# Performance work log

Hardware: AMD Instinct MI355X
Metric: run time of the kernel (lower is better)

## Reference

```python
import jax, jax.numpy as jnp
import numpy as np

DEPTH = 6
GAMMA = 1e-4
DIM = 1024
HIDDEN = 16
OUT_DIM = 64
N = 16384


def setup_inputs() -> dict:
    key = jax.random.key(0)
    k0, k1, k2, k3, k4 = jax.random.split(key, 5)
    X = jax.random.normal(k0, (N, DIM), dtype=jnp.float32)
    s1 = 1.0 / np.sqrt(DIM)
    s2 = 1.0 / np.sqrt(HIDDEN)
    W1 = jax.random.uniform(k1, (DIM, HIDDEN), jnp.float32, -s1, s1)
    b1 = jax.random.uniform(k2, (HIDDEN,), jnp.float32, -s1, s1)
    W2 = jax.random.uniform(k3, (HIDDEN, OUT_DIM), jnp.float32, -s2, s2)
    b2 = jax.random.uniform(k4, (OUT_DIM,), jnp.float32, -s2, s2)
    return {"X": X, "W1": W1, "b1": b1, "W2": W2, "b2": b2}


def _mlp(X, W1, b1, W2, b2):
    # shared FeedForwardClassifier: Linear(dim,16) -> ReLU -> Linear(16,out_dim)
    return jax.nn.relu(X @ W1 + b1) @ W2 + b2


def reference(X, W1, b1, W2, b2):
    for _ in range(DEPTH):
        # custom LayerNorm: row-wise L2 normalization (no eps in original)
        Xn = X / jnp.linalg.norm(X, axis=-1, keepdims=True)  # [N, dim]
        P = jax.nn.softmax(_mlp(Xn, W1, b1, W2, b2), axis=-1)  # [N, out_dim]
        # X + g*P@P.T@X - g*X@X.T@X, contracted small-Gram-first (same math)
        PtX = P.T @ Xn          # [out_dim, dim]
        G = Xn.T @ Xn           # [dim, dim]
        X = Xn + GAMMA * (P @ PtX) - GAMMA * (Xn @ G)
    return _mlp(X, W1, b1, W2, b2)
```

## Files before the change

### kernel.cpp

```cpp
#include <hip/hip_runtime.h>


#define N_ROWS 16384
#define DIM 1024
#define HID 16
#define OUTD 64
#define DEPTH 6
#define GAMMA 1e-4f

typedef short bf16x8 __attribute__((ext_vector_type(8)));
typedef unsigned short u16x8 __attribute__((ext_vector_type(8)));
typedef float f32x4 __attribute__((ext_vector_type(4)));

#define AS1C(p) ((const __attribute__((address_space(1))) void*)(p))
#define AS3(p)  ((__attribute__((address_space(3))) void*)(p))

__device__ __forceinline__ unsigned short f2bf(float f) {
    unsigned u = __builtin_bit_cast(unsigned, f);
    u += 0x7fffu + ((u >> 16) & 1u);
    return (unsigned short)(u >> 16);
}
__device__ __forceinline__ float b2f(ushort u) {
    unsigned x = ((unsigned)u) << 16;
    return __builtin_bit_cast(float, x);
}
__device__ __forceinline__ int swz(int n, int row) {
    return (n & ~63) | ((((n >> 3) & 7) ^ (row & 7)) << 3) | (n & 7);
}

__device__ __forceinline__ void atom_pk_bf16(ushort* p, ushort lo, ushort hi) {
#if __has_builtin(__builtin_amdgcn_global_atomic_fadd_v2bf16)
    typedef short s16x2 __attribute__((ext_vector_type(2)));
    s16x2 v;
    v[0] = (short)lo; v[1] = (short)hi;
    __builtin_amdgcn_global_atomic_fadd_v2bf16(
        (__attribute__((address_space(1))) s16x2*)p, v);
#else
    unsigned* up = (unsigned*)p;
    unsigned expected = *up;
    while (true) {
        float flo = b2f((ushort)(expected & 0xffffu)) + b2f(lo);
        float fhi = b2f((ushort)(expected >> 16)) + b2f(hi);
        unsigned desired = (unsigned)f2bf(flo) | ((unsigned)f2bf(fhi) << 16);
        unsigned old = atomicCAS(up, expected, desired);
        if (old == expected) break;
        expected = old;
    }
#endif
}

__global__ __launch_bounds__(256) void tobf16_k(const float* __restrict__ X,
        ushort* __restrict__ Xm, float* __restrict__ rinv) {
    int row = blockIdx.x, t = threadIdx.x;
    float4 v = ((const float4*)(X + (size_t)row * DIM))[t];
    ushort4 o4;
    o4.x = f2bf(v.x); o4.y = f2bf(v.y); o4.z = f2bf(v.z); o4.w = f2bf(v.w);
    *(ushort4*)(Xm + (size_t)row * DIM + swz(t * 4, row)) = o4;
    float ss = v.x * v.x + v.y * v.y + v.z * v.z + v.w * v.w;
    for (int o = 32; o > 0; o >>= 1) ss += __shfl_down(ss, o);
    __shared__ float wsum[4];
    if ((t & 63) == 0) wsum[t >> 6] = ss;
    __syncthreads();
    if (t == 0) rinv[row] = 1.0f / sqrtf(wsum[0] + wsum[1] + wsum[2] + wsum[3]);
}

__global__ __launch_bounds__(256) void rsqrt_k(const float* __restrict__ ssacc,
        float* __restrict__ rinv) {
    int i = blockIdx.x * 256 + threadIdx.x;
    rinv[i] = 1.0f / sqrtf(ssacc[i]);
}

__global__ __launch_bounds__(256) void transpose_k(const ushort* __restrict__ Xm,
        const float* __restrict__ rinv, ushort* __restrict__ XnT) {
    int r0 = blockIdx.x * 64;
    int c0 = blockIdx.y * 64;
    int t = threadIdx.x;
    __shared__ float ts[64 * 65];
    __shared__ float riS[64];
    if (t < 64) riS[t] = rinv[r0 + t];
    __syncthreads();
#pragma unroll
    for (int i = 0; i < 2; ++i) {
        int idx = i * 256 + t;
        int r = idx >> 3, lg = idx & 7;
        int rr = r0 + r;
        const ushort* p = Xm + (size_t)rr * DIM + c0 + ((lg ^ (rr & 7)) << 3);
        u16x8 a = *(const u16x8*)p;
        float s = riS[r];
        float* d = &ts[r * 65 + lg * 8];
#pragma unroll
        for (int u = 0; u < 8; ++u) d[u] = b2f(a[u]) * s;
    }
    __syncthreads();
#pragma unroll
    for (int i = 0; i < 2; ++i) {
        int g = i * 256 + t;
        int c = g >> 3;
        int rg = g & 7;
        u16x8 pk;
#pragma unroll
        for (int u = 0; u < 8; ++u) pk[u] = f2bf(ts[(rg * 8 + u) * 65 + c]);
        *(u16x8*)(XnT + (size_t)(c0 + c) * N_ROWS + r0 + ((rg ^ (c & 7)) << 3)) = pk;
    }
}

__global__ __launch_bounds__(256) void prep_w1t_k(const float* __restrict__ W1,
        ushort* __restrict__ W1T) {
    int idx = blockIdx.x * 256 + threadIdx.x;
    int h = idx >> 10, j = idx & 1023;
    W1T[idx] = f2bf(W1[j * HID + h]);
}

__global__ __launch_bounds__(256) void zgemm_k(const ushort* __restrict__ Xm,
        const ushort* __restrict__ W1T, const float* __restrict__ b1,
        float* __restrict__ z, const float* __restrict__ rv) {
    int t = threadIdx.x;
    int wave = t >> 6, lane = t & 63;
    int rl = lane & 15, q = lane >> 4;
    int rowbase = blockIdx.x * 64 + wave * 16;
    int m = rowbase + rl;
    int msw = m & 7;
    const ushort* arow = Xm + (size_t)m * DIM;
    const ushort* brow = W1T + (size_t)rl * DIM + q * 8;
    f32x4 acc = {0.f, 0.f, 0.f, 0.f};
#pragma unroll 8
    for (int kt = 0; kt < DIM; kt += 32) {
        int gl = ((kt >> 3) & 7) | q;
        int off = (kt & ~63) + ((gl ^ msw) << 3);
        bf16x8 a = *(const bf16x8*)(arow + off);
        bf16x8 b = *(const bf16x8*)(brow + kt);
        acc = __builtin_amdgcn_mfma_f32_16x16x32_bf16(a, b, acc, 0, 0, 0);
    }
#pragma unroll
    for (int rg = 0; rg < 4; ++rg) {
        int mm = rowbase + q * 4 + rg;
        float s = rv ? rv[mm] : 1.0f;
        z[(size_t)mm * HID + rl] = acc[rg] * s + b1[rl];
    }
}

__global__ __launch_bounds__(256) void head_k(const float* __restrict__ z,
        const float* __restrict__ W2, const float* __restrict__ b2,
        ushort* __restrict__ Pb, ushort* __restrict__ PTb,
        float* __restrict__ out, int do_softmax) {
    __shared__ float w2s[HID * OUTD];
    __shared__ float b2s[OUTD];
    int t = threadIdx.x;
    ((float4*)w2s)[t] = ((const float4*)W2)[t];
    if (t < OUTD) b2s[t] = b2[t];
    __syncthreads();
    int m = blockIdx.x * 256 + t;
    float h[HID];
    const float4* zp = (const float4*)(z + (size_t)m * HID);
#pragma unroll
    for (int i = 0; i < 4; ++i) {
        float4 v = zp[i];
        h[i * 4 + 0] = fmaxf(v.x, 0.f); h[i * 4 + 1] = fmaxf(v.y, 0.f);
        h[i * 4 + 2] = fmaxf(v.z, 0.f); h[i * 4 + 3] = fmaxf(v.w, 0.f);
    }
    float lo[OUTD];
#pragma unroll
    for (int o = 0; o < OUTD; ++o) lo[o] = b2s[o];
    for (int i = 0; i < HID; ++i) {
        float hv = h[i];
#pragma unroll
        for (int o = 0; o < OUTD; ++o) lo[o] += hv * w2s[i * OUTD + o];
    }
    if (do_softmax) {
        float mx = lo[0];
#pragma unroll
        for (int o = 1; o < OUTD; ++o) mx = fmaxf(mx, lo[o]);
        float sm = 0.f;
#pragma unroll
        for (int o = 0; o < OUTD; ++o) { float e = __expf(lo[o] - mx); lo[o] = e; sm += e; }
        float inv = 1.0f / sm;
#pragma unroll
        for (int o8 = 0; o8 < 8; ++o8) {
            u16x8 pk;
#pragma unroll
            for (int u = 0; u < 8; ++u) pk[u] = f2bf(lo[o8 * 8 + u] * inv);
            ((u16x8*)(Pb + (size_t)m * OUTD))[o8 ^ (m & 7)] = pk;
        }
#pragma unroll
        for (int o = 0; o < OUTD; ++o)
            PTb[(size_t)o * N_ROWS + swz(m, o)] = f2bf(lo[o] * inv);
    } else {
        float4* op = (float4*)(out + (size_t)m * OUTD);
#pragma unroll
        for (int o4 = 0; o4 < 16; ++o4) {
            float4 v; v.x = lo[o4 * 4 + 0]; v.y = lo[o4 * 4 + 1];
            v.z = lo[o4 * 4 + 2]; v.w = lo[o4 * 4 + 3];
            op[o4] = v;
        }
    }
}

__global__ __launch_bounds__(256) void castgp_k(const ushort* __restrict__ Gacc,
        const ushort* __restrict__ PtXacc, ushort* __restrict__ Gb,
        ushort* __restrict__ PtXTb) {
    int idx = blockIdx.x * 256 + threadIdx.x;
    if (idx < 262144) {
        int n = idx >> 8;
        int so = (idx & 255) * 4;
        int k0 = (so & ~63) | ((((so >> 3) & 7) ^ (n & 7)) << 3) | (so & 7);
        ushort4 o;
        ushort v0 = (k0 + 0 > n) ? Gacc[(size_t)n * DIM + k0 + 0] : Gacc[(size_t)(k0 + 0) * DIM + n];
        ushort v1 = (k0 + 1 > n) ? Gacc[(size_t)n * DIM + k0 + 1] : Gacc[(size_t)(k0 + 1) * DIM + n];
        ushort v2 = (k0 + 2 > n) ? Gacc[(size_t)n * DIM + k0 + 2] : Gacc[(size_t)(k0 + 2) * DIM + n];
        ushort v3 = (k0 + 3 > n) ? Gacc[(size_t)n * DIM + k0 + 3] : Gacc[(size_t)(k0 + 3) * DIM + n];
        o.x = v0 ^ 0x8000u; o.y = v1 ^ 0x8000u;
        o.z = v2 ^ 0x8000u; o.w = v3 ^ 0x8000u;
        *(ushort4*)(Gb + (size_t)n * DIM + so) = o;
    } else {
        int vv = idx - 262144;
        int d = vv >> 4;
        int so = (vv & 15) * 4;
        int k0 = ((((so >> 3) & 7) ^ (d & 7)) << 3) | (so & 7);
        const ushort* src = PtXacc + (size_t)d * OUTD + k0;
        ushort4 o;
        o.x = src[0]; o.y = src[1]; o.z = src[2]; o.w = src[3];
        *(ushort4*)(PtXTb + (size_t)d * OUTD + so) = o;
    }
}

template<int BM, int BN, int EPI, int TRI>
__global__ __launch_bounds__(256, 3) void gemm_nt_k(
        const ushort* __restrict__ A0, int lda0,
        const ushort* __restrict__ B0, int ldb0, int k0len,
        const ushort* __restrict__ A1, int lda1,
        const ushort* __restrict__ B1, int ldb1, int k1len,
        float* __restrict__ C, int ldc,
        const float* __restrict__ rinv, float gamma,
        float* __restrict__ ssacc) {
    constexpr int WTN = BN / 2;
    constexpr int NF = WTN / 16;
    constexpr int NAW = BM / 64;
    constexpr int NBW = BN / 64;
    __shared__ ushort ls[(BM + BN) * 64];
    ushort* lsA = ls;
    ushort* lsB = ls + BM * 64;
    int t = threadIdx.x;
    int wave = t >> 6, lane = t & 63;
    int rl = lane & 15, q = lane >> 4;
    int wm = wave & 1, wn = wave >> 1;
    int m0, n0, zidx;
    if (TRI) {
        int bid = blockIdx.x;
        int rest = bid >> 3;
        int bx = rest % 36, tm = 0;
        int zhi = rest / 36;
        zidx = (bid & 7) | (zhi << 3);
        while (bx >= 8 - tm) { bx -= 8 - tm; ++tm; }
        m0 = tm * 128; n0 = (tm + bx) * 128;
    } else {
        m0 = blockIdx.x * BM; n0 = blockIdx.y * BN; zidx = blockIdx.z;
    }
    int lrow8 = lane >> 3, lgrp = lane & 7;
    bool isA = wave < NAW;
    bool active = wave < NAW + NBW;
    int wlocal = isA ? wave : wave - NAW;
    ushort* dstb = ls + (isA ? 0 : BM * 64) + wlocal * 4096;

    f32x4 acc[4][NF];
#pragma unroll
    for (int i = 0; i < 4; ++i)
#pragma unroll
        for (int j = 0; j < NF; ++j) acc[i][j] = f32x4{0.f, 0.f, 0.f, 0.f};
    float rvv[4][4];

    for (int seg = 0; seg < 2; ++seg) {
        int klen = seg ? k1len : k0len;
        if (klen > 0) {
            const ushort* OPA = seg ? A1 : A0;
            const ushort* OPB = seg ? B1 : B0;
            int ldaS = seg ? lda1 : lda0;
            int ldbS = seg ? ldb1 : ldb0;
            int kb = seg ? 0 : zidx * k0len;
            const ushort* srcb;
            size_t ldS;
            if (isA) {
                srcb = OPA + (size_t)(m0 + wlocal * 64 + lrow8) * ldaS + lgrp * 8;
                ldS = (size_t)ldaS;
            } else {
                srcb = OPB + (size_t)(n0 + wlocal * 64 + lrow8) * ldbS + lgrp * 8;
                ldS = (size_t)ldbS;
            }
            srcb += kb;
            for (int kt = 0; kt < klen; kt += 64) {
                if (active) {
#pragma unroll
                    for (int c = 0; c < 8; ++c)
                        __builtin_amdgcn_global_load_lds(AS1C(srcb + c * 8 * ldS),
                                                         AS3(dstb + c * 512), 16, 0, 0);
                    srcb += 64;
                }
                __syncthreads();
#pragma unroll
                for (int s = 0; s < 2; ++s) {
                    bf16x8 af[4], bfr[NF];
#pragma unroll
                    for (int i = 0; i < 4; ++i) {
                        int row = wm * 64 + i * 16 + rl;
                        int sg = ((s << 2) | q) ^ (row & 7);
                        af[i] = *(const bf16x8*)&lsA[row * 64 + sg * 8];
                    }
#pragma unroll
                    for (int j = 0; j < NF; ++j) {
                        int row = wn * WTN + j * 16 + rl;
                        int sg = ((s << 2) | q) ^ (row & 7);
                        bfr[j] = *(const bf16x8*)&lsB[row * 64 + sg * 8];
                    }
#pragma unroll
                    for (int i = 0; i < 4; ++i)
#pragma unroll
                        for (int j = 0; j < NF; ++j)
                            acc[i][j] = __builtin_amdgcn_mfma_f32_16x16x32_bf16(
                                af[i], bfr[j], acc[i][j], 0, 0, 0);
                }
                __syncthreads();
            }
        }
        if (EPI == 1 && seg == 0) {
#pragma unroll
            for (int i = 0; i < 4; ++i)
#pragma unroll
                for (int rg = 0; rg < 4; ++rg)
                    rvv[i][rg] = rinv[m0 + wm * 64 + i * 16 + q * 4 + rg];
#pragma unroll
            for (int i = 0; i < 4; ++i)
#pragma unroll
                for (int j = 0; j < NF; ++j)
#pragma unroll
                    for (int rg = 0; rg < 4; ++rg)
                        acc[i][j][rg] *= rvv[i][rg];
        }
    }

    if (EPI == 0) {
        ushort* Cb = (ushort*)C;
#pragma unroll
        for (int i = 0; i < 4; ++i)
#pragma unroll
            for (int j = 0; j < NF; ++j)
#pragma unroll
                for (int rg = 0; rg < 4; ++rg) {
                    int m = m0 + wm * 64 + i * 16 + q * 4 + rg;
                    int n = n0 + wn * WTN + j * 16 + rl;
                    float v = acc[i][j][rg];
                    float vp = __shfl_xor(v, 1);
                    if ((rl & 1) == 0)
                        atom_pk_bf16(&Cb[(size_t)m * ldc + n], f2bf(v), f2bf(vp));
                }
    } else {
#pragma unroll
        for (int i = 0; i < 4; ++i)
#pragma unroll
            for (int rg = 0; rg < 4; ++rg) {
                int m = m0 + wm * 64 + i * 16 + q * 4 + rg;
                float ssl = 0.f;
#pragma unroll
                for (int j = 0; j < NF; ++j) {
                    int n = n0 + wn * WTN + j * 16 + rl;
                    int so = swz(n, m);
                    float base = b2f(A0[(size_t)m * lda0 + so]);
                    float vf = base * rvv[i][rg] + gamma * acc[i][j][rg];
                    ((ushort*)C)[(size_t)m * ldc + so] = f2bf(vf);
                    ssl += vf * vf;
                }
                ssl += __shfl_xor(ssl, 1);
                ssl += __shfl_xor(ssl, 2);
                ssl += __shfl_xor(ssl, 4);
                ssl += __shfl_xor(ssl, 8);
                if (rl == 0) atomicAdd(&ssacc[m], ssl);
            }
    }
}

extern "C" void kernel_launch(void* const* d_in, const int* in_sizes, int n_in,
                              void* d_out, int out_size, void* d_ws, size_t ws_size,
                              hipStream_t stream) {
    const float* X = (const float*)d_in[0];
    const float* W1 = (const float*)d_in[1];
    const float* b1 = (const float*)d_in[2];
    const float* W2 = (const float*)d_in[3];
    const float* b2 = (const float*)d_in[4];
    float* out = (float*)d_out;
    char* ws = (char*)d_ws;

    constexpr size_t O_BufA  = 0;
    constexpr size_t O_BufB  = O_BufA + (size_t)N_ROWS * DIM * 2;
    constexpr size_t O_Pb    = O_BufB + (size_t)N_ROWS * DIM * 2;
    constexpr size_t O_PTb   = O_Pb + (size_t)N_ROWS * OUTD * 2;
    constexpr size_t O_Gacc  = O_PTb + (size_t)OUTD * N_ROWS * 2;
    constexpr size_t O_PXacc = O_Gacc + (size_t)DIM * DIM * 2;
    constexpr size_t O_ssacc = O_PXacc + (size_t)DIM * OUTD * 2;
    constexpr size_t O_Gb    = O_ssacc + (size_t)N_ROWS * 4;
    constexpr size_t O_PtXTb = O_Gb + (size_t)DIM * DIM * 2;
    constexpr size_t O_riv   = O_PtXTb + (size_t)DIM * OUTD * 2;
    constexpr size_t O_z     = O_riv + (size_t)N_ROWS * 4;
    constexpr size_t O_W1T   = O_z + (size_t)N_ROWS * HID * 4;

    ushort* bufA  = (ushort*)(ws + O_BufA);
    ushort* bufB  = (ushort*)(ws + O_BufB);
    ushort* Pb    = (ushort*)(ws + O_Pb);
    ushort* PTb   = (ushort*)(ws + O_PTb);
    ushort* Gacc  = (ushort*)(ws + O_Gacc);
    ushort* PXacc = (ushort*)(ws + O_PXacc);
    float*  ssacc = (float*)(ws + O_ssacc);
    ushort* Gb    = (ushort*)(ws + O_Gb);
    ushort* PtXTb = (ushort*)(ws + O_PtXTb);
    float*  riv   = (float*)(ws + O_riv);
    float*  z     = (float*)(ws + O_z);
    ushort* W1T   = (ushort*)(ws + O_W1T);
    (void)in_sizes; (void)n_in; (void)out_size; (void)ws_size;

    prep_w1t_k<<<64, 256, 0, stream>>>(W1, W1T);
    tobf16_k<<<N_ROWS, 256, 0, stream>>>(X, bufA, riv);

    ushort* xm  = bufA;
    ushort* alt = bufB;

    for (int it = 0; it < DEPTH; ++it) {
        transpose_k<<<dim3(N_ROWS / 64, DIM / 64), 256, 0, stream>>>(xm, riv, alt);
        zgemm_k<<<N_ROWS / 64, 256, 0, stream>>>(xm, W1T, b1, z, riv);
        head_k<<<N_ROWS / 256, 256, 0, stream>>>(z, W2, b2, Pb, PTb, nullptr, 1);
        hipMemsetAsync(ws + O_Gacc, 0,
                       (size_t)DIM * DIM * 2 + (size_t)DIM * OUTD * 2
                       + (size_t)N_ROWS * 4, stream);
        gemm_nt_k<128, 128, 0, 1><<<dim3(8 * 36 * 2, 1, 1), 256, 0, stream>>>(
            alt, N_ROWS, alt, N_ROWS, 1024,
            nullptr, 0, nullptr, 0, 0,
            (float*)Gacc, DIM, nullptr, 0.f, nullptr);
        gemm_nt_k<128, 64, 0, 0><<<dim3(8, 1, 64), 256, 0, stream>>>(
            alt, N_ROWS, PTb, N_ROWS, 256,
            nullptr, 0, nullptr, 0, 0,
            (float*)PXacc, OUTD, nullptr, 0.f, nullptr);
        castgp_k<<<1088, 256, 0, stream>>>(Gacc, PXacc, Gb, PtXTb);
        gemm_nt_k<128, 128, 1, 0><<<dim3(N_ROWS / 128, DIM / 128, 1), 256, 0, stream>>>(
            xm, DIM, Gb, DIM, 1024,
            Pb, OUTD, PtXTb, OUTD, OUTD,
            (float*)alt, DIM, riv, GAMMA, ssacc);
        rsqrt_k<<<N_ROWS / 256, 256, 0, stream>>>(ssacc, riv);
        ushort* tmp = xm; xm = alt; alt = tmp;
    }

    zgemm_k<<<N_ROWS / 64, 256, 0, stream>>>(xm, W1T, b1, z, nullptr);
    head_k<<<N_ROWS / 256, 256, 0, stream>>>(z, W2, b2, Pb, PTb, out, 0);
}
```

Before: 1.088 ms.

## Merge Gram and PᵀX GEMMs into one launch and fuse zeroing into rsqrt

Replaces the two split-K accumulation GEMMs (XᵀX triangle and PᵀX) with one kernel launch of 1088 blocks, padding PT to 128 rows so both use 128x128 tiles. The per-iteration memset is removed: the rsqrt kernel now also clears ssacc and the Gacc/PXacc accumulators, and an initial memset covers the first iteration. The z buffer is aliased onto Gb. The goal is fewer launches and better load balance across one combined grid. The cost is extra padded PᵀX work, and correctness now depends on the aliasing and zeroing order.

Measured after the change: 1.129 ms. +3.7%, slower.

```diff
diff --git a/kernel.cpp b/kernel.cpp
--- a/kernel.cpp
+++ b/kernel.cpp
@@ -64,10 +64,14 @@
     if (t == 0) rinv[row] = 1.0f / sqrtf(wsum[0] + wsum[1] + wsum[2] + wsum[3]);
 }
 
-__global__ __launch_bounds__(256) void rsqrt_k(const float* __restrict__ ssacc,
-        float* __restrict__ rinv) {
+__global__ __launch_bounds__(256) void rsqrt_zero_k(float* __restrict__ ssacc,
+        float* __restrict__ rinv, uint4* __restrict__ gz) {
     int i = blockIdx.x * 256 + threadIdx.x;
-    rinv[i] = 1.0f / sqrtf(ssacc[i]);
+    if (i < N_ROWS) {
+        rinv[i] = 1.0f / sqrtf(ssacc[i]);
+        ssacc[i] = 0.f;
+    }
+    gz[i] = uint4{0u, 0u, 0u, 0u};
 }
 
 __global__ __launch_bounds__(256) void transpose_k(const ushort* __restrict__ Xm,
@@ -196,7 +200,7 @@
 }
 
 __global__ __launch_bounds__(256) void castgp_k(const ushort* __restrict__ Gacc,
-        const ushort* __restrict__ PtXacc, ushort* __restrict__ Gb,
+        const ushort* __restrict__ PXacc, ushort* __restrict__ Gb,
         ushort* __restrict__ PtXTb) {
     int idx = blockIdx.x * 256 + threadIdx.x;
     if (idx < 262144) {
@@ -216,111 +220,178 @@
         int d = vv >> 4;
         int so = (vv & 15) * 4;
         int k0 = ((((so >> 3) & 7) ^ (d & 7)) << 3) | (so & 7);
-        const ushort* src = PtXacc + (size_t)d * OUTD + k0;
+        const ushort* src = PXacc + (size_t)d * 128 + k0;
         ushort4 o;
         o.x = src[0]; o.y = src[1]; o.z = src[2]; o.w = src[3];
         *(ushort4*)(PtXTb + (size_t)d * OUTD + so) = o;
     }
 }
 
-template<int BM, int BN, int EPI, int TRI>
-__global__ __launch_bounds__(256, 3) void gemm_nt_k(
+__global__ __launch_bounds__(256, 3) void gemm_gp_k(
+        const ushort* __restrict__ XnT, const ushort* __restrict__ PTpad,
+        ushort* __restrict__ Gacc, ushort* __restrict__ PXacc) {
+    __shared__ ushort ls[256 * 64];
+    ushort* lsA = ls;
+    ushort* lsB = ls + 128 * 64;
+    int t = threadIdx.x;
+    int wave = t >> 6, lane = t & 63;
+    int rl = lane & 15, q = lane >> 4;
+    int wm = wave & 1, wn = wave >> 1;
+    int bid = blockIdx.x;
+    int m0, n0, kb, ksteps, ldc;
+    const ushort* B;
+    ushort* C;
+    if (bid < 576) {
+        int rest = bid >> 3;
+        int bx = rest % 36, zhi = rest / 36, tm = 0;
+        int zidx = (bid & 7) | (zhi << 3);
+        while (bx >= 8 - tm) { bx -= 8 - tm; ++tm; }
+        m0 = tm * 128; n0 = (tm + bx) * 128;
+        kb = zidx * 1024; ksteps = 16;
+        B = XnT; C = Gacc; ldc = DIM;
+    } else {
+        int b2 = bid - 576;
+        int zidx = b2 & 63;
+        m0 = (b2 >> 6) * 128; n0 = 0;
+        kb = zidx * 256; ksteps = 4;
+        B = PTpad; C = PXacc; ldc = 128;
+    }
+    int lrow8 = lane >> 3, lgrp = lane & 7;
+    bool isA = wave < 2;
+    int wlocal = wave & 1;
+    ushort* dstb = ls + (isA ? 0 : 8192) + wlocal * 4096;
+    const ushort* srcb = (isA
+        ? XnT + (size_t)(m0 + wlocal * 64 + lrow8) * N_ROWS
+        : B   + (size_t)(n0 + wlocal * 64 + lrow8) * N_ROWS) + kb + lgrp * 8;
+
+    f32x4 acc[4][4];
+#pragma unroll
+    for (int i = 0; i < 4; ++i)
+#pragma unroll
+        for (int j = 0; j < 4; ++j) acc[i][j] = f32x4{0.f, 0.f, 0.f, 0.f};
+
+    for (int st = 0; st < ksteps; ++st) {
+#pragma unroll
+        for (int c = 0; c < 8; ++c)
+            __builtin_amdgcn_global_load_lds(AS1C(srcb + (size_t)c * 8 * N_ROWS),
+                                             AS3(dstb + c * 512), 16, 0, 0);
+        srcb += 64;
+        __syncthreads();
+#pragma unroll
+        for (int s = 0; s < 2; ++s) {
+            bf16x8 af[4], bfr[4];
+#pragma unroll
+            for (int i = 0; i < 4; ++i) {
+                int row = wm * 64 + i * 16 + rl;
+                int sg = ((s << 2) | q) ^ (row & 7);
+                af[i] = *(const bf16x8*)&lsA[row * 64 + sg * 8];
+            }
+#pragma unroll
+            for (int j = 0; j < 4; ++j) {
+                int row = wn * 64 + j * 16 + rl;
+                int sg = ((s << 2) | q) ^ (row & 7);
+                bfr[j] = *(const bf16x8*)&lsB[row * 64 + sg * 8];
+            }
+#pragma unroll
+            for (int i = 0; i < 4; ++i)
+#pragma unroll
+                for (int j = 0; j < 4; ++j)
+                    acc[i][j] = __builtin_amdgcn_mfma_f32_16x16x32_bf16(
+                        af[i], bfr[j], acc[i][j], 0, 0, 0);
+        }
+        __syncthreads();
+    }
+
+#pragma unroll
+    for (int i = 0; i < 4; ++i)
+#pragma unroll
+        for (int j = 0; j < 4; ++j)
+#pragma unroll
+            for (int rg = 0; rg < 4; ++rg) {
+                int m = m0 + wm * 64 + i * 16 + q * 4 + rg;
+                int n = n0 + wn * 64 + j * 16 + rl;
+                float v = acc[i][j][rg];
+                float vp = __shfl_xor(v, 1);
+                if ((rl & 1) == 0)
+                    atom_pk_bf16(&C[(size_t)m * ldc + n], f2bf(v), f2bf(vp));
+            }
+}
+
+__global__ __launch_bounds__(256, 3) void gemm_upd_k(
         const ushort* __restrict__ A0, int lda0,
         const ushort* __restrict__ B0, int ldb0, int k0len,
         const ushort* __restrict__ A1, int lda1,
         const ushort* __restrict__ B1, int ldb1, int k1len,
-        float* __restrict__ C, int ldc,
+        ushort* __restrict__ C, int ldc,
         const float* __restrict__ rinv, float gamma,
         float* __restrict__ ssacc) {
-    constexpr int WTN = BN / 2;
-    constexpr int NF = WTN / 16;
-    constexpr int NAW = BM / 64;
-    constexpr int NBW = BN / 64;
-    __shared__ ushort ls[(BM + BN) * 64];
+    __shared__ ushort ls[256 * 64];
     ushort* lsA = ls;
-    ushort* lsB = ls + BM * 64;
+    ushort* lsB = ls + 128 * 64;
     int t = threadIdx.x;
     int wave = t >> 6, lane = t & 63;
     int rl = lane & 15, q = lane >> 4;
     int wm = wave & 1, wn = wave >> 1;
-    int m0, n0, zidx;
-    if (TRI) {
-        int bid = blockIdx.x;
-        int rest = bid >> 3;
-        int bx = rest % 36, tm = 0;
-        int zhi = rest / 36;
-        zidx = (bid & 7) | (zhi << 3);
-        while (bx >= 8 - tm) { bx -= 8 - tm; ++tm; }
-        m0 = tm * 128; n0 = (tm + bx) * 128;
-    } else {
-        m0 = blockIdx.x * BM; n0 = blockIdx.y * BN; zidx = blockIdx.z;
-    }
+    int m0 = blockIdx.x * 128, n0 = blockIdx.y * 128;
     int lrow8 = lane >> 3, lgrp = lane & 7;
-    bool isA = wave < NAW;
-    bool active = wave < NAW + NBW;
-    int wlocal = isA ? wave : wave - NAW;
-    ushort* dstb = ls + (isA ? 0 : BM * 64) + wlocal * 4096;
-
-    f32x4 acc[4][NF];
+    bool isA = wave < 2;
+    int wlocal = wave & 1;
+    ushort* dstb = ls + (isA ? 0 : 8192) + wlocal * 4096;
+
+    f32x4 acc[4][4];
 #pragma unroll
     for (int i = 0; i < 4; ++i)
 #pragma unroll
-        for (int j = 0; j < NF; ++j) acc[i][j] = f32x4{0.f, 0.f, 0.f, 0.f};
+        for (int j = 0; j < 4; ++j) acc[i][j] = f32x4{0.f, 0.f, 0.f, 0.f};
     float rvv[4][4];
 
     for (int seg = 0; seg < 2; ++seg) {
         int klen = seg ? k1len : k0len;
-        if (klen > 0) {
-            const ushort* OPA = seg ? A1 : A0;
-            const ushort* OPB = seg ? B1 : B0;
-            int ldaS = seg ? lda1 : lda0;
-            int ldbS = seg ? ldb1 : ldb0;
-            int kb = seg ? 0 : zidx * k0len;
-            const ushort* srcb;
-            size_t ldS;
-            if (isA) {
-                srcb = OPA + (size_t)(m0 + wlocal * 64 + lrow8) * ldaS + lgrp * 8;
-                ldS = (size_t)ldaS;
-            } else {
-                srcb = OPB + (size_t)(n0 + wlocal * 64 + lrow8) * ldbS + lgrp * 8;
-                ldS = (size_t)ldbS;
+        const ushort* OPA = seg ? A1 : A0;
+        const ushort* OPB = seg ? B1 : B0;
+        int ldaS = seg ? lda1 : lda0;
+        int ldbS = seg ? ldb1 : ldb0;
+        const ushort* srcb;
+        size_t ldS;
+        if (isA) {
+            srcb = OPA + (size_t)(m0 + wlocal * 64 + lrow8) * ldaS + lgrp * 8;
+            ldS = (size_t)ldaS;
+        } else {
+            srcb = OPB + (size_t)(n0 + wlocal * 64 + lrow8) * ldbS + lgrp * 8;
+            ldS = (size_t)ldbS;
+        }
+        for (int kt = 0; kt < klen; kt += 64) {
+#pragma unroll
+            for (int c = 0; c < 8; ++c)
+                __builtin_amdgcn_global_load_lds(AS1C(srcb + c * 8 * ldS),
+                                                 AS3(dstb + c * 512), 16, 0, 0);
+            srcb += 64;
+            __syncthreads();
+#pragma unroll
+            for (int s = 0; s < 2; ++s) {
+                bf16x8 af[4], bfr[4];
+#pragma unroll
+                for (int i = 0; i < 4; ++i) {
+                    int row = wm * 64 + i * 16 + rl;
+                    int sg = ((s << 2) | q) ^ (row & 7);
+                    af[i] = *(const bf16x8*)&lsA[row * 64 + sg * 8];
+                }
+#pragma unroll
+                for (int j = 0; j < 4; ++j) {
+                    int row = wn * 64 + j * 16 + rl;
+                    int sg = ((s << 2) | q) ^ (row & 7);
+                    bfr[j] = *(const bf16x8*)&lsB[row * 64 + sg * 8];
+                }
+#pragma unroll
+                for (int i = 0; i < 4; ++i)
+#pragma unroll
+                    for (int j = 0; j < 4; ++j)
+                        acc[i][j] = __builtin_amdgcn_mfma_f32_16x16x32_bf16(
+                            af[i], bfr[j], acc[i][j], 0, 0, 0);
             }
-            srcb += kb;
-            for (int kt = 0; kt < klen; kt += 64) {
-                if (active) {
-#pragma unroll
-                    for (int c = 0; c < 8; ++c)
-                        __builtin_amdgcn_global_load_lds(AS1C(srcb + c * 8 * ldS),
-                                                         AS3(dstb + c * 512), 16, 0, 0);
-                    srcb += 64;
-                }
-                __syncthreads();
-#pragma unroll
-                for (int s = 0; s < 2; ++s) {
-                    bf16x8 af[4], bfr[NF];
-#pragma unroll
-                    for (int i = 0; i < 4; ++i) {
-                        int row = wm * 64 + i * 16 + rl;
-                        int sg = ((s << 2) | q) ^ (row & 7);
-                        af[i] = *(const bf16x8*)&lsA[row * 64 + sg * 8];
-                    }
-#pragma unroll
-                    for (int j = 0; j < NF; ++j) {
-                        int row = wn * WTN + j * 16 + rl;
-                        int sg = ((s << 2) | q) ^ (row & 7);
-                        bfr[j] = *(const bf16x8*)&lsB[row * 64 + sg * 8];
-                    }
-#pragma unroll
-                    for (int i = 0; i < 4; ++i)
-#pragma unroll
-                        for (int j = 0; j < NF; ++j)
-                            acc[i][j] = __builtin_amdgcn_mfma_f32_16x16x32_bf16(
-                                af[i], bfr[j], acc[i][j], 0, 0, 0);
-                }
-                __syncthreads();
-            }
-        }
-        if (EPI == 1 && seg == 0) {
+            __syncthreads();
+        }
+        if (seg == 0) {
 #pragma unroll
             for (int i = 0; i < 4; ++i)
 #pragma unroll
@@ -329,51 +400,34 @@
 #pragma unroll
             for (int i = 0; i < 4; ++i)
 #pragma unroll
-                for (int j = 0; j < NF; ++j)
+                for (int j = 0; j < 4; ++j)
 #pragma unroll
                     for (int rg = 0; rg < 4; ++rg)
                         acc[i][j][rg] *= rvv[i][rg];
         }
     }
 
-    if (EPI == 0) {
-        ushort* Cb = (ushort*)C;
-#pragma unroll
-        for (int i = 0; i < 4; ++i)
-#pragma unroll
-            for (int j = 0; j < NF; ++j)
-#pragma unroll
-                for (int rg = 0; rg < 4; ++rg) {
-                    int m = m0 + wm * 64 + i * 16 + q * 4 + rg;
-                    int n = n0 + wn * WTN + j * 16 + rl;
-                    float v = acc[i][j][rg];
-                    float vp = __shfl_xor(v, 1);
-                    if ((rl & 1) == 0)
-                        atom_pk_bf16(&Cb[(size_t)m * ldc + n], f2bf(v), f2bf(vp));
-                }
-    } else {
-#pragma unroll
-        for (int i = 0; i < 4; ++i)
-#pragma unroll
-            for (int rg = 0; rg < 4; ++rg) {
-                int m = m0 + wm * 64 + i * 16 + q * 4 + rg;
-                float ssl = 0.f;
-#pragma unroll
-                for (int j = 0; j < NF; ++j) {
-                    int n = n0 + wn * WTN + j * 16 + rl;
-                    int so = swz(n, m);
-                    float base = b2f(A0[(size_t)m * lda0 + so]);
-                    float vf = base * rvv[i][rg] + gamma * acc[i][j][rg];
-                    ((ushort*)C)[(size_t)m * ldc + so] = f2bf(vf);
-                    ssl += vf * vf;
-                }
-                ssl += __shfl_xor(ssl, 1);
-                ssl += __shfl_xor(ssl, 2);
-                ssl += __shfl_xor(ssl, 4);
-                ssl += __shfl_xor(ssl, 8);
-                if (rl == 0) atomicAdd(&ssacc[m], ssl);
+#pragma unroll
+    for (int i = 0; i < 4; ++i)
+#pragma unroll
+        for (int rg = 0; rg < 4; ++rg) {
+            int m = m0 + wm * 64 + i * 16 + q * 4 + rg;
+            float ssl = 0.f;
+#pragma unroll
+            for (int j = 0; j < 4; ++j) {
+                int n = n0 + wn * 64 + j * 16 + rl;
+                int so = swz(n, m);
+                float base = b2f(A0[(size_t)m * lda0 + so]);
+                float vf = base * rvv[i][rg] + gamma * acc[i][j][rg];
+                C[(size_t)m * ldc + so] = f2bf(vf);
+                ssl += vf * vf;
             }
-    }
+            ssl += __shfl_xor(ssl, 1);
+            ssl += __shfl_xor(ssl, 2);
+            ssl += __shfl_xor(ssl, 4);
+            ssl += __shfl_xor(ssl, 8);
+            if (rl == 0) atomicAdd(&ssacc[m], ssl);
+        }
 }
 
 extern "C" void kernel_launch(void* const* d_in, const int* in_sizes, int n_in,
@@ -391,14 +445,13 @@
     constexpr size_t O_BufB  = O_BufA + (size_t)N_ROWS * DIM * 2;
     constexpr size_t O_Pb    = O_BufB + (size_t)N_ROWS * DIM * 2;
     constexpr size_t O_PTb   = O_Pb + (size_t)N_ROWS * OUTD * 2;
-    constexpr size_t O_Gacc  = O_PTb + (size_t)OUTD * N_ROWS * 2;
+    constexpr size_t O_Gacc  = O_PTb + (size_t)128 * N_ROWS * 2;
     constexpr size_t O_PXacc = O_Gacc + (size_t)DIM * DIM * 2;
-    constexpr size_t O_ssacc = O_PXacc + (size_t)DIM * OUTD * 2;
+    constexpr size_t O_ssacc = O_PXacc + (size_t)DIM * 128 * 2;
     constexpr size_t O_Gb    = O_ssacc + (size_t)N_ROWS * 4;
     constexpr size_t O_PtXTb = O_Gb + (size_t)DIM * DIM * 2;
     constexpr size_t O_riv   = O_PtXTb + (size_t)DIM * OUTD * 2;
-    constexpr size_t O_z     = O_riv + (size_t)N_ROWS * 4;
-    constexpr size_t O_W1T   = O_z + (size_t)N_ROWS * HID * 4;
+    constexpr size_t O_W1T   = O_riv + (size_t)N_ROWS * 4;
 
     ushort* bufA  = (ushort*)(ws + O_BufA);
     ushort* bufB  = (ushort*)(ws + O_BufB);
@@ -408,14 +461,17 @@
     ushort* PXacc = (ushort*)(ws + O_PXacc);
     float*  ssacc = (float*)(ws + O_ssacc);
     ushort* Gb    = (ushort*)(ws + O_Gb);
+    float*  z     = (float*)(ws + O_Gb);
     ushort* PtXTb = (ushort*)(ws + O_PtXTb);
     float*  riv   = (float*)(ws + O_riv);
-    float*  z     = (float*)(ws + O_z);
     ushort* W1T   = (ushort*)(ws + O_W1T);
     (void)in_sizes; (void)n_in; (void)out_size; (void)ws_size;
 
     prep_w1t_k<<<64, 256, 0, stream>>>(W1, W1T);
     tobf16_k<<<N_ROWS, 256, 0, stream>>>(X, bufA, riv);
+    hipMemsetAsync(ws + O_PTb + (size_t)OUTD * N_ROWS * 2, 0,
+                   (size_t)OUTD * N_ROWS * 2 + (size_t)DIM * DIM * 2
+                   + (size_t)DIM * 128 * 2 + (size_t)N_ROWS * 4, stream);
 
     ushort* xm  = bufA;
     ushort* alt = bufB;
@@ -424,23 +480,13 @@
         transpose_k<<<dim3(N_ROWS / 64, DIM / 64), 256, 0, stream>>>(xm, riv, alt);
         zgemm_k<<<N_ROWS / 64, 256, 0, stream>>>(xm, W1T, b1, z, riv);
         head_k<<<N_ROWS / 256, 256, 0, stream>>>(z, W2, b2, Pb, PTb, nullptr, 1);
-        hipMemsetAsync(ws + O_Gacc, 0,
-                       (size_t)DIM * DIM * 2 + (size_t)DIM * OUTD * 2
-                       + (size_t)N_ROWS * 4, stream);
-        gemm_nt_k<128, 128, 0, 1><<<dim3(8 * 36 * 2, 1, 1), 256, 0, stream>>>(
-            alt, N_ROWS, alt, N_ROWS, 1024,
-            nullptr, 0, nullptr, 0, 0,
-            (float*)Gacc, DIM, nullptr, 0.f, nullptr);
-        gemm_nt_k<128, 64, 0, 0><<<dim3(8, 1, 64), 256, 0, stream>>>(
-            alt, N_ROWS, PTb, N_ROWS, 256,
-            nullptr, 0, nullptr, 0, 0,
-            (float*)PXacc, OUTD, nullptr, 0.f, nullptr);
+        gemm_gp_k<<<1088, 256, 0, stream>>>(alt, PTb, Gacc, PXacc);
         castgp_k<<<1088, 256, 0, stream>>>(Gacc, PXacc, Gb, PtXTb);
-        gemm_nt_k<128, 128, 1, 0><<<dim3(N_ROWS / 128, DIM / 128, 1), 256, 0, stream>>>(
+        gemm_upd_k<<<dim3(N_ROWS / 128, DIM / 128), 256, 0, stream>>>(
             xm, DIM, Gb, DIM, 1024,
             Pb, OUTD, PtXTb, OUTD, OUTD,
-            (float*)alt, DIM, riv, GAMMA, ssacc);
-        rsqrt_k<<<N_ROWS / 256, 256, 0, stream>>>(ssacc, riv);
+            alt, DIM, riv, GAMMA, ssacc);
+        rsqrt_zero_k<<<576, 256, 0, stream>>>(ssacc, riv, (uint4*)(ws + O_Gacc));
         ushort* tmp = xm; xm = alt; alt = tmp;
     }
 
```
